# Performance work log

Measured on AMD Instinct MI355X. Metric: run time of the kernel, lower is better.

## Reference

```python
import jax, jax.numpy as jnp
import numpy as np
from itertools import product

N_BOARD = 11          # Hex board size from docstring
N_OUT = N_BOARD + 1   # 12
BATCH = 32768

PATTERNS = jnp.asarray(list(product([-1, 0, 1], repeat=3)), dtype=jnp.float32)  # (27, 3)


def setup_inputs() -> dict:
    key = jax.random.key(0)
    # ternary board values in {-1, 0, 1}
    boards = jax.random.randint(key, (BATCH, N_BOARD, N_BOARD), 0, 3).astype(jnp.float32) - 1.0
    return {"boards": boards}


def _encode(boards):
    b = boards.shape[0]
    n = boards.shape[-1] + 1  # 12
    # pad to (n+1)x(n+1)=13x13 with 0, then border fill: top/bottom rows = 1, left/right cols = -1
    P = jnp.pad(boards, ((0, 0), (1, 1), (1, 1)))
    P = P.at[:, 0, 1:-1].set(1.0).at[:, -1, 1:-1].set(1.0)
    P = P.at[:, 1:-1, 0].set(-1.0).at[:, 1:-1, -1].set(-1.0)
    # 2x2 window flattened -> first 3 elems: a0=P[i,j], a1=P[i,j+1], a2=P[i+1,j]; each (b, n, n)
    a0 = P[:, :-1, :-1]
    a1 = P[:, :-1, 1:]
    a2 = P[:, 1:, :-1]
    # compare each element against the 27 patterns -> (b, 27, n, n)
    eq0 = a0[:, None] == PATTERNS[None, :, 0, None, None]
    eq1 = a1[:, None] == PATTERNS[None, :, 1, None, None]
    eq2 = a2[:, None] == PATTERNS[None, :, 2, None, None]
    # corner wildcards: at (0,0) pattern elem 0 is forced equal; (0,n-1) elem 1; (n-1,0) elem 2
    eq0 = eq0.at[:, :, 0, 0].set(True)
    eq1 = eq1.at[:, :, 0, n - 1].set(True)
    eq2 = eq2.at[:, :, n - 1, 0].set(True)
    return (eq0 & eq1 & eq2).astype(jnp.float32)  # (b, 27, n, n)


def reference(boards):
    return _encode(boards)
```

## Files before the change

### kernel.cpp

```cpp
#include <hip/hip_runtime.h>


#define G 8

typedef float f4 __attribute__((ext_vector_type(4)));

__global__ __launch_bounds__(256) void hex_encode_kernel(
    const float* __restrict__ boards, float* __restrict__ out)
{
    __shared__ float sP[G][169];
    __shared__ __align__(16) unsigned short sMask[G][144];
    __shared__ unsigned sNeed[27];

    const int tid = threadIdx.x;
    const size_t b0 = (size_t)blockIdx.x * G;

    if (tid < 27) {
        int v0 = tid / 9, v1 = (tid / 3) % 3, v2 = tid % 3;
        sNeed[tid] = (1u << v0) | (1u << (3 + v1)) | (1u << (6 + v2));
    }

    #pragma unroll
    for (int it = 0; it < 6; ++it) {
        int idx = tid + it * 256;
        if (idx < G * 169) {
            int g = idx / 169;
            int pos = idx - g * 169;
            int pr = pos / 13, pc = pos % 13;
            bool ir = (pr >= 1) & (pr <= 11);
            bool jr = (pc >= 1) & (pc <= 11);
            float v;
            if (ir & jr)  v = boards[(b0 + g) * 121 + (pr - 1) * 11 + (pc - 1)];
            else if (jr)  v = 1.0f;
            else if (ir)  v = -1.0f;
            else          v = 0.0f;
            sP[g][pos] = v;
        }
    }
    __syncthreads();

    #pragma unroll
    for (int it = 0; it < 5; ++it) {
        int idx = tid + it * 256;
        if (idx < G * 144) {
            int g = idx / 144;
            int cell = idx - g * 144;
            int r = cell / 12, c = cell % 12;
            const float* P = sP[g];
            int i0 = (int)P[r * 13 + c] + 1;
            int i1 = (int)P[r * 13 + c + 1] + 1;
            int i2 = (int)P[(r + 1) * 13 + c] + 1;
            unsigned m0 = (cell == 0)   ? 7u : (1u << i0);
            unsigned m1 = (cell == 11)  ? 7u : (1u << i1);
            unsigned m2 = (cell == 132) ? 7u : (1u << i2);
            sMask[g][cell] = (unsigned short)(m0 | (m1 << 3) | (m2 << 6));
        }
    }
    __syncthreads();

    f4* outv = (f4*)out + b0 * 972;
    const unsigned long long* mask64 = (const unsigned long long*)sMask;
    for (int it = 0; it < 31; ++it) {
        int idx = tid + it * 256;
        if (idx < G * 972) {
            int g = idx / 972;
            int rem = idx - g * 972;
            int p = rem / 36;
            int cell4 = rem - p * 36;
            unsigned need = sNeed[p];
            unsigned long long m4 = mask64[g * 36 + cell4];
            f4 o;
            o.x = (((unsigned)(m4)       & need) == need) ? 1.0f : 0.0f;
            o.y = (((unsigned)(m4 >> 16) & need) == need) ? 1.0f : 0.0f;
            o.z = (((unsigned)(m4 >> 32) & need) == need) ? 1.0f : 0.0f;
            o.w = (((unsigned)(m4 >> 48) & need) == need) ? 1.0f : 0.0f;
            __builtin_nontemporal_store(o, &outv[idx]);
        }
    }
}

extern "C" void kernel_launch(void* const* d_in, const int* in_sizes, int n_in,
                              void* d_out, int out_size, void* d_ws, size_t ws_size,
                              hipStream_t stream) {
    const float* boards = (const float*)d_in[0];
    float* out = (float*)d_out;
    hex_encode_kernel<<<32768 / G, 256, 0, stream>>>(boards, out);
}
```

Measured before the change: 106.5 us.

## Split encoding into mask-building kernel and pure output-streaming kernel

```diff
diff --git a/kernel.cpp b/kernel.cpp
--- a/kernel.cpp
+++ b/kernel.cpp
@@ -5,20 +5,19 @@
 
 typedef float f4 __attribute__((ext_vector_type(4)));
 
-__global__ __launch_bounds__(256) void hex_encode_kernel(
-    const float* __restrict__ boards, float* __restrict__ out)
+__constant__ unsigned c_need[27] = {
+    73, 137, 265, 81, 145, 273, 97, 161, 289,
+    74, 138, 266, 82, 146, 274, 98, 162, 290,
+    76, 140, 268, 84, 148, 276, 100, 164, 292};
+
+__global__ __launch_bounds__(256) void mask_kernel(
+    const float* __restrict__ boards, unsigned long long* __restrict__ ws)
 {
     __shared__ float sP[G][169];
     __shared__ __align__(16) unsigned short sMask[G][144];
-    __shared__ unsigned sNeed[27];
 
     const int tid = threadIdx.x;
     const size_t b0 = (size_t)blockIdx.x * G;
-
-    if (tid < 27) {
-        int v0 = tid / 9, v1 = (tid / 3) % 3, v2 = tid % 3;
-        sNeed[tid] = (1u << v0) | (1u << (3 + v1)) | (1u << (6 + v2));
-    }
 
     #pragma unroll
     for (int it = 0; it < 6; ++it) {
@@ -58,23 +57,34 @@
     }
     __syncthreads();
 
-    f4* outv = (f4*)out + b0 * 972;
-    const unsigned long long* mask64 = (const unsigned long long*)sMask;
-    for (int it = 0; it < 31; ++it) {
+    if (tid < G * 18) {
+        ((ulonglong2*)(ws + (size_t)blockIdx.x * (G * 36)))[tid] =
+            ((const ulonglong2*)sMask)[tid];
+    }
+}
+
+__global__ __launch_bounds__(256) void stream_kernel(
+    const unsigned long long* __restrict__ masks, float* __restrict__ out)
+{
+    const int tid = threadIdx.x;
+    const size_t b = blockIdx.x;
+    const unsigned long long* mb = masks + b * 36;
+    f4* outv = (f4*)out + b * 972;
+
+    #pragma unroll
+    for (int it = 0; it < 4; ++it) {
         int idx = tid + it * 256;
-        if (idx < G * 972) {
-            int g = idx / 972;
-            int rem = idx - g * 972;
-            int p = rem / 36;
-            int cell4 = rem - p * 36;
-            unsigned need = sNeed[p];
-            unsigned long long m4 = mask64[g * 36 + cell4];
+        if (idx < 972) {
+            int p = idx / 36;
+            int cell4 = idx - p * 36;
+            unsigned need = c_need[p];
+            unsigned long long m4 = mb[cell4];
             f4 o;
             o.x = (((unsigned)(m4)       & need) == need) ? 1.0f : 0.0f;
             o.y = (((unsigned)(m4 >> 16) & need) == need) ? 1.0f : 0.0f;
             o.z = (((unsigned)(m4 >> 32) & need) == need) ? 1.0f : 0.0f;
             o.w = (((unsigned)(m4 >> 48) & need) == need) ? 1.0f : 0.0f;
-            __builtin_nontemporal_store(o, &outv[idx]);
+            outv[idx] = o;
         }
     }
 }
@@ -84,5 +94,7 @@
                               hipStream_t stream) {
     const float* boards = (const float*)d_in[0];
     float* out = (float*)d_out;
-    hex_encode_kernel<<<32768 / G, 256, 0, stream>>>(boards, out);
+    unsigned long long* ws = (unsigned long long*)d_ws;
+    mask_kernel<<<32768 / G, 256, 0, stream>>>(boards, ws);
+    stream_kernel<<<32768, 256, 0, stream>>>(ws, out);
 }
```

After: 118.8 us. 11.5% more time.

## Process boards per wave with wave barriers and register prefetch of next board

Applied to the files above, without the earlier changes.

```diff
diff --git a/kernel.cpp b/kernel.cpp
--- a/kernel.cpp
+++ b/kernel.cpp
@@ -1,80 +1,99 @@
 #include <hip/hip_runtime.h>
 
 
-#define G 8
+typedef float f4 __attribute__((ext_vector_type(4)));
 
-typedef float f4 __attribute__((ext_vector_type(4)));
+#define NBLOCK 2048
+#define BOARDS_PER_WAVE 4
 
 __global__ __launch_bounds__(256) void hex_encode_kernel(
     const float* __restrict__ boards, float* __restrict__ out)
 {
-    __shared__ float sP[G][169];
-    __shared__ __align__(16) unsigned short sMask[G][144];
+    __shared__ float sP[4][176];
+    __shared__ __align__(8) unsigned short sMask[4][160];
     __shared__ unsigned sNeed[27];
 
     const int tid = threadIdx.x;
-    const size_t b0 = (size_t)blockIdx.x * G;
+    const int wave = tid >> 6;
+    const int lane = tid & 63;
 
     if (tid < 27) {
         int v0 = tid / 9, v1 = (tid / 3) % 3, v2 = tid % 3;
         sNeed[tid] = (1u << v0) | (1u << (3 + v1)) | (1u << (6 + v2));
     }
 
+    float* P = sP[wave];
+    unsigned short* M = sMask[wave];
+
     #pragma unroll
-    for (int it = 0; it < 6; ++it) {
-        int idx = tid + it * 256;
-        if (idx < G * 169) {
-            int g = idx / 169;
-            int pos = idx - g * 169;
-            int pr = pos / 13, pc = pos % 13;
+    for (int s = 0; s < 3; ++s) {
+        int j = lane + s * 64;
+        if (j < 169) {
+            int pr = j / 13, pc = j % 13;
             bool ir = (pr >= 1) & (pr <= 11);
             bool jr = (pc >= 1) & (pc <= 11);
-            float v;
-            if (ir & jr)  v = boards[(b0 + g) * 121 + (pr - 1) * 11 + (pc - 1)];
-            else if (jr)  v = 1.0f;
-            else if (ir)  v = -1.0f;
-            else          v = 0.0f;
-            sP[g][pos] = v;
+            if (!(ir & jr))
+                P[j] = jr ? 1.0f : (ir ? -1.0f : 0.0f);
         }
     }
     __syncthreads();
 
-    #pragma unroll
-    for (int it = 0; it < 5; ++it) {
-        int idx = tid + it * 256;
-        if (idx < G * 144) {
-            int g = idx / 144;
-            int cell = idx - g * 144;
-            int r = cell / 12, c = cell % 12;
-            const float* P = sP[g];
-            int i0 = (int)P[r * 13 + c] + 1;
-            int i1 = (int)P[r * 13 + c + 1] + 1;
-            int i2 = (int)P[(r + 1) * 13 + c] + 1;
-            unsigned m0 = (cell == 0)   ? 7u : (1u << i0);
-            unsigned m1 = (cell == 11)  ? 7u : (1u << i1);
-            unsigned m2 = (cell == 132) ? 7u : (1u << i2);
-            sMask[g][cell] = (unsigned short)(m0 | (m1 << 3) | (m2 << 6));
+    const size_t wgid = (size_t)blockIdx.x * 4 + wave;
+    const size_t b0 = wgid * BOARDS_PER_WAVE;
+
+    const float* bp = boards + b0 * 121;
+    float r0 = bp[lane];
+    float r1 = (lane < 57) ? bp[64 + lane] : 0.0f;
+
+    for (int k = 0; k < BOARDS_PER_WAVE; ++k) {
+        const size_t b = b0 + k;
+
+        P[(1 + lane / 11) * 13 + 1 + lane % 11] = r0;
+        if (lane < 57)
+            P[(1 + (lane + 64) / 11) * 13 + 1 + (lane + 64) % 11] = r1;
+        asm volatile("s_waitcnt lgkmcnt(0)" ::: "memory");
+        __builtin_amdgcn_wave_barrier();
+
+        #pragma unroll
+        for (int s = 0; s < 3; ++s) {
+            int j = lane + s * 64;
+            if (j < 144) {
+                int r = j / 12, c = j - 12 * r;
+                int i0 = (int)P[r * 13 + c] + 1;
+                int i1 = (int)P[r * 13 + c + 1] + 1;
+                int i2 = (int)P[(r + 1) * 13 + c] + 1;
+                unsigned m0 = (j == 0)   ? 7u : (1u << i0);
+                unsigned m1 = (j == 11)  ? 7u : (1u << i1);
+                unsigned m2 = (j == 132) ? 7u : (1u << i2);
+                M[j] = (unsigned short)(m0 | (m1 << 3) | (m2 << 6));
+            }
         }
-    }
-    __syncthreads();
+        asm volatile("s_waitcnt lgkmcnt(0)" ::: "memory");
+        __builtin_amdgcn_wave_barrier();
 
-    f4* outv = (f4*)out + b0 * 972;
-    const unsigned long long* mask64 = (const unsigned long long*)sMask;
-    for (int it = 0; it < 31; ++it) {
-        int idx = tid + it * 256;
-        if (idx < G * 972) {
-            int g = idx / 972;
-            int rem = idx - g * 972;
-            int p = rem / 36;
-            int cell4 = rem - p * 36;
-            unsigned need = sNeed[p];
-            unsigned long long m4 = mask64[g * 36 + cell4];
-            f4 o;
-            o.x = (((unsigned)(m4)       & need) == need) ? 1.0f : 0.0f;
-            o.y = (((unsigned)(m4 >> 16) & need) == need) ? 1.0f : 0.0f;
-            o.z = (((unsigned)(m4 >> 32) & need) == need) ? 1.0f : 0.0f;
-            o.w = (((unsigned)(m4 >> 48) & need) == need) ? 1.0f : 0.0f;
-            __builtin_nontemporal_store(o, &outv[idx]);
+        if (k + 1 < BOARDS_PER_WAVE) {
+            const float* np = boards + (b + 1) * 121;
+            r0 = np[lane];
+            r1 = (lane < 57) ? np[64 + lane] : 0.0f;
+        }
+
+        f4* outv = (f4*)out + b * 972;
+        const unsigned long long* m64 = (const unsigned long long*)M;
+        #pragma unroll 4
+        for (int it = 0; it < 16; ++it) {
+            int idx = lane + it * 64;
+            if (idx < 972) {
+                int p = idx / 36;
+                int cell4 = idx - p * 36;
+                unsigned need = sNeed[p];
+                unsigned long long m4 = m64[cell4];
+                f4 o;
+                o.x = (((unsigned)(m4)       & need) == need) ? 1.0f : 0.0f;
+                o.y = (((unsigned)(m4 >> 16) & need) == need) ? 1.0f : 0.0f;
+                o.z = (((unsigned)(m4 >> 32) & need) == need) ? 1.0f : 0.0f;
+                o.w = (((unsigned)(m4 >> 48) & need) == need) ? 1.0f : 0.0f;
+                outv[idx] = o;
+            }
         }
     }
 }
@@ -84,5 +103,5 @@
                               hipStream_t stream) {
     const float* boards = (const float*)d_in[0];
     float* out = (float*)d_out;
-    hex_encode_kernel<<<32768 / G, 256, 0, stream>>>(boards, out);
+    hex_encode_kernel<<<NBLOCK, 256, 0, stream>>>(boards, out);
 }
```

Result: slower. 111.8 us (+4.9%).
